# Kernel optimization log

Measured on AMD Instinct MI355X. Metric: run time of the kernel, lower is better.

Reference implementation:

```python
import jax, jax.numpy as jnp
import numpy as np

T, H, W = 365, 256, 256
IN_SZ, HID, OUT_SZ = 2, 64, 1
H_SCALE = 0.1


def setup_inputs() -> dict:
    key = jax.random.key(0)
    ks = jax.random.split(key, 9)
    lim_ih = 1.0 / np.sqrt(HID)
    return {
        "precipitation": jax.random.uniform(ks[0], (T, H, W), dtype=jnp.float32),
        "temperature": jax.random.normal(ks[1], (T, H, W), dtype=jnp.float32),
        "weight_ih": jax.random.uniform(ks[2], (3 * HID, IN_SZ), minval=-lim_ih, maxval=lim_ih, dtype=jnp.float32),
        "weight_hh": jax.random.uniform(ks[3], (3 * HID, HID), minval=-lim_ih, maxval=lim_ih, dtype=jnp.float32),
        "bias": jax.random.uniform(ks[4], (3 * HID,), minval=-lim_ih, maxval=lim_ih, dtype=jnp.float32),
        "bias_n": jax.random.uniform(ks[5], (HID,), minval=-lim_ih, maxval=lim_ih, dtype=jnp.float32),
        "out_w": jax.random.uniform(ks[6], (OUT_SZ, HID), minval=-lim_ih, maxval=lim_ih, dtype=jnp.float32),
        "out_b": jax.random.uniform(ks[7], (OUT_SZ,), minval=-lim_ih, maxval=lim_ih, dtype=jnp.float32),
        "init_h": jax.random.normal(ks[8], (HID,), dtype=jnp.float32) * H_SCALE,
    }


def reference(precipitation, temperature, weight_ih, weight_hh, bias, bias_n, out_w, out_b, init_h):
    t, h, w = temperature.shape
    # (T, N, 2) with N = H*W grid cells treated as batch
    inputs = jnp.stack([precipitation, temperature], axis=-1).reshape(t, h * w, -1)
    h0 = jnp.broadcast_to(init_h, (h * w, init_h.shape[0]))

    def step(hidden, x_t):
        igates = x_t @ weight_ih.T + bias          # (N, 3*HID)
        hgates = hidden @ weight_hh.T              # (N, 3*HID)
        ir, iz, in_ = jnp.split(igates, 3, axis=-1)
        hr, hz, hn = jnp.split(hgates, 3, axis=-1)
        reset = jax.nn.sigmoid(ir + hr)
        update = jax.nn.sigmoid(iz + hz)
        new = jnp.tanh(in_ + reset * (hn + bias_n))
        h_next = new + update * (hidden - new)    # equinox GRUCell convention
        y = (h_next @ out_w.T + out_b)[..., 0]    # (N,)
        return h_next, y

    final_h_flat, smb_flat = jax.lax.scan(step, h0, inputs)
    smb = smb_flat.reshape(t, h, w)
    final_h = final_h_flat.reshape(h, w, -1)
    return smb, final_h
```

## Files before the change

kernel.cpp:

```cpp
#include <hip/hip_runtime.h>

#define T_STEPS 365
#define NCELLS  65536

typedef __attribute__((ext_vector_type(8))) short short8;
typedef __attribute__((ext_vector_type(4))) float f32x4;

static __device__ __forceinline__ short f2bf_rne(float x) {
    union { float f; unsigned u; } v; v.f = x;
    unsigned r = v.u + 0x7fffu + ((v.u >> 16) & 1u);
    return (short)(r >> 16);
}
static __device__ __forceinline__ float bf2f(short b) {
    union { float f; unsigned u; } v; v.u = ((unsigned)(unsigned short)b) << 16;
    return v.f;
}
static __device__ __forceinline__ float fast_rcp(float x) { return __builtin_amdgcn_rcpf(x); }

__global__ __launch_bounds__(256, 2)
void gru_mfma_kernel(const float* __restrict__ precip,
                     const float* __restrict__ temp,
                     const float* __restrict__ w_ih,
                     const float* __restrict__ w_hh,
                     const float* __restrict__ bias,
                     const float* __restrict__ bias_n,
                     const float* __restrict__ out_w,
                     const float* __restrict__ out_b,
                     const float* __restrict__ init_h,
                     float* __restrict__ out)
{
    __shared__ float hbuf[4][16][68];

    const int lane = threadIdx.x & 63;
    const int wid  = threadIdx.x >> 6;
    const int c    = lane & 15;
    const int q    = lane >> 4;
    const int base = (blockIdx.x * 4 + wid) * 16;

    short8 Bf[12][2];
#pragma unroll
    for (int jt = 0; jt < 12; ++jt)
#pragma unroll
        for (int f = 0; f < 2; ++f) {
            const float* src = w_hh + ((16 * jt + c) * 64 + 32 * f + 8 * q);
#pragma unroll
            for (int e = 0; e < 8; ++e) Bf[jt][f][e] = f2bf_rne(src[e]);
        }

    float wr0[4], wr1[4], wz0[4], wz1[4], wn0[4], wn1[4];
    float br[4], bz[4], bn_[4], bnn[4], ow[4];
#pragma unroll
    for (int j = 0; j < 4; ++j) {
        const int u = 16 * j + c;
        wr0[j] = w_ih[2 * u];       wr1[j] = w_ih[2 * u + 1];
        wz0[j] = w_ih[128 + 2 * u]; wz1[j] = w_ih[129 + 2 * u];
        wn0[j] = w_ih[256 + 2 * u]; wn1[j] = w_ih[257 + 2 * u];
        br[j]  = bias[u]; bz[j] = bias[64 + u]; bn_[j] = bias[128 + u];
        bnn[j] = bias_n[u]; ow[j] = out_w[u];
    }
    const float ob = out_b[0];

    float hC[4][4];
#pragma unroll
    for (int j = 0; j < 4; ++j) {
        const float iv = init_h[16 * j + c];
#pragma unroll
        for (int reg = 0; reg < 4; ++reg) hC[j][reg] = iv;
    }
#pragma unroll
    for (int j = 0; j < 4; ++j)
#pragma unroll
        for (int reg = 0; reg < 4; ++reg)
            hbuf[wid][4 * q + reg][16 * j + c] = hC[j][reg];

    const bool selb0 = (c & 1), selb1 = (c & 2);
    const bool do_store = (c < 4);

#pragma unroll 1
    for (int t = 0; t < T_STEPS; ++t) {
        const size_t tofs = (size_t)t * NCELLS + base;
        float pv[4], tv[4];
#pragma unroll
        for (int reg = 0; reg < 4; ++reg) {
            pv[reg] = precip[tofs + 4 * q + reg];
            tv[reg] = temp  [tofs + 4 * q + reg];
        }

        const float* row = &hbuf[wid][c][0];
        f32x4 a0 = *(const f32x4*)(row + 8 * q);
        f32x4 a1 = *(const f32x4*)(row + 8 * q + 4);
        f32x4 a2 = *(const f32x4*)(row + 32 + 8 * q);
        f32x4 a3 = *(const f32x4*)(row + 32 + 8 * q + 4);
        short8 ah0, al0, ah1, al1;
#pragma unroll
        for (int e = 0; e < 4; ++e) {
            short h0 = f2bf_rne(a0[e]); ah0[e]     = h0; al0[e]     = f2bf_rne(a0[e] - bf2f(h0));
            short h1 = f2bf_rne(a1[e]); ah0[4 + e] = h1; al0[4 + e] = f2bf_rne(a1[e] - bf2f(h1));
            short h2 = f2bf_rne(a2[e]); ah1[e]     = h2; al1[e]     = f2bf_rne(a2[e] - bf2f(h2));
            short h3 = f2bf_rne(a3[e]); ah1[4 + e] = h3; al1[4 + e] = f2bf_rne(a3[e] - bf2f(h3));
        }

        f32x4 acc[12];
#pragma unroll
        for (int jt = 0; jt < 12; ++jt) {
            f32x4 a = {0.f, 0.f, 0.f, 0.f};
            a = __builtin_amdgcn_mfma_f32_16x16x32_bf16(ah0, Bf[jt][0], a, 0, 0, 0);
            a = __builtin_amdgcn_mfma_f32_16x16x32_bf16(ah1, Bf[jt][1], a, 0, 0, 0);
            a = __builtin_amdgcn_mfma_f32_16x16x32_bf16(al0, Bf[jt][0], a, 0, 0, 0);
            a = __builtin_amdgcn_mfma_f32_16x16x32_bf16(al1, Bf[jt][1], a, 0, 0, 0);
            acc[jt] = a;
        }

        float psum[4] = {0.f, 0.f, 0.f, 0.f};
#pragma unroll
        for (int j = 0; j < 4; ++j) {
#pragma unroll
            for (int reg = 0; reg < 4; ++reg) {
                const float hr = acc[j][reg];
                const float hz = acc[4 + j][reg];
                const float hn = acc[8 + j][reg];
                const float ir = fmaf(wr0[j], pv[reg], fmaf(wr1[j], tv[reg], br[j]));
                const float iz = fmaf(wz0[j], pv[reg], fmaf(wz1[j], tv[reg], bz[j]));
                const float in_= fmaf(wn0[j], pv[reg], fmaf(wn1[j], tv[reg], bn_[j]));
                const float r  = fast_rcp(1.f + __expf(-(ir + hr)));
                const float z  = fast_rcp(1.f + __expf(-(iz + hz)));
                const float a_ = fmaf(r, hn + bnn[j], in_);
                const float th = 1.f - 2.f * fast_rcp(1.f + __expf(a_ + a_));
                const float hnew = fmaf(z, hC[j][reg] - th, th);
                hC[j][reg] = hnew;
                psum[reg] = fmaf(hnew, ow[j], psum[reg]);
            }
        }

#pragma unroll
        for (int j = 0; j < 4; ++j)
#pragma unroll
            for (int reg = 0; reg < 4; ++reg)
                hbuf[wid][4 * q + reg][16 * j + c] = hC[j][reg];

#pragma unroll
        for (int reg = 0; reg < 4; ++reg) {
            psum[reg] += __shfl_xor(psum[reg], 1);
            psum[reg] += __shfl_xor(psum[reg], 2);
            psum[reg] += __shfl_xor(psum[reg], 4);
            psum[reg] += __shfl_xor(psum[reg], 8);
        }
        float ya = selb0 ? psum[1] : psum[0];
        float yb = selb0 ? psum[3] : psum[2];
        float yv = selb1 ? yb : ya;
        if (do_store) out[tofs + 4 * q + c] = yv + ob;
    }

    const size_t fofs = (size_t)T_STEPS * NCELLS + (size_t)base * 64;
#pragma unroll
    for (int j = 0; j < 4; ++j)
#pragma unroll
        for (int reg = 0; reg < 4; ++reg)
            out[fofs + (size_t)(4 * q + reg) * 64 + 16 * j + c] = hC[j][reg];
}

extern "C" void kernel_launch(void* const* d_in, const int* in_sizes, int n_in,
                              void* d_out, int out_size, void* d_ws, size_t ws_size,
                              hipStream_t stream) {
    const float* precip = (const float*)d_in[0];
    const float* temp   = (const float*)d_in[1];
    const float* w_ih   = (const float*)d_in[2];
    const float* w_hh   = (const float*)d_in[3];
    const float* bias   = (const float*)d_in[4];
    const float* bias_n = (const float*)d_in[5];
    const float* out_w  = (const float*)d_in[6];
    const float* out_b  = (const float*)d_in[7];
    const float* init_h = (const float*)d_in[8];

    gru_mfma_kernel<<<NCELLS / 64, 256, 0, stream>>>(
        precip, temp, w_ih, w_hh, bias, bias_n, out_w, out_b, init_h,
        (float*)d_out);
}
```

Before: 2.405 ms.

## Move W_hh fragments to LDS and fold input gates into MFMA

The W_hh bf16 fragments are no longer held in registers. They are now read each step from shared memory, which frees VGPRs so launch bounds can ask for 3 blocks per SM instead of 2. The r and z input projections plus their biases are folded into an extra MFMA per tile. It uses an augmented A operand (precip/temp hi-lo split and a constant 1.0) with a packed B of w_ih and a bias hi/lo pair, replacing per-element FMAs. The cost is extra LDS reads and one extra MFMA per r/z tile each timestep, plus some precision change from bf16 splitting of the input weights.

```diff
diff --git a/kernel.cpp b/kernel.cpp
--- a/kernel.cpp
+++ b/kernel.cpp
@@ -5,6 +5,7 @@
 
 typedef __attribute__((ext_vector_type(8))) short short8;
 typedef __attribute__((ext_vector_type(4))) float f32x4;
+typedef __attribute__((ext_vector_type(4))) unsigned int u32x4;
 
 static __device__ __forceinline__ short f2bf_rne(float x) {
     union { float f; unsigned u; } v; v.f = x;
@@ -15,9 +16,12 @@
     union { float f; unsigned u; } v; v.u = ((unsigned)(unsigned short)b) << 16;
     return v.f;
 }
+static __device__ __forceinline__ unsigned pack2(short lo, short hi) {
+    return ((unsigned)(unsigned short)lo) | (((unsigned)(unsigned short)hi) << 16);
+}
 static __device__ __forceinline__ float fast_rcp(float x) { return __builtin_amdgcn_rcpf(x); }
 
-__global__ __launch_bounds__(256, 2)
+__global__ __launch_bounds__(256, 3)
 void gru_mfma_kernel(const float* __restrict__ precip,
                      const float* __restrict__ temp,
                      const float* __restrict__ w_ih,
@@ -29,34 +33,48 @@
                      const float* __restrict__ init_h,
                      float* __restrict__ out)
 {
+    __shared__ u32x4 Bfrag[1536];
+    __shared__ u32x4 BExt[256];
     __shared__ float hbuf[4][16][68];
 
-    const int lane = threadIdx.x & 63;
-    const int wid  = threadIdx.x >> 6;
+    const int tid  = threadIdx.x;
+    const int lane = tid & 63;
+    const int wid  = tid >> 6;
     const int c    = lane & 15;
     const int q    = lane >> 4;
     const int base = (blockIdx.x * 4 + wid) * 16;
 
-    short8 Bf[12][2];
-#pragma unroll
-    for (int jt = 0; jt < 12; ++jt)
-#pragma unroll
-        for (int f = 0; f < 2; ++f) {
-            const float* src = w_hh + ((16 * jt + c) * 64 + 32 * f + 8 * q);
-#pragma unroll
-            for (int e = 0; e < 8; ++e) Bf[jt][f][e] = f2bf_rne(src[e]);
-        }
-
-    float wr0[4], wr1[4], wz0[4], wz1[4], wn0[4], wn1[4];
-    float br[4], bz[4], bn_[4], bnn[4], ow[4];
+    for (int idx = tid; idx < 1536; idx += 256) {
+        const int l = idx & 63, jtf = idx >> 6;
+        const int jt = jtf >> 1, f = jtf & 1;
+        const float* src = w_hh + ((16 * jt + (l & 15)) * 64 + 32 * f + 8 * (l >> 4));
+        u32x4 d;
+#pragma unroll
+        for (int p2 = 0; p2 < 4; ++p2)
+            d[p2] = pack2(f2bf_rne(src[2 * p2]), f2bf_rne(src[2 * p2 + 1]));
+        Bfrag[idx] = d;
+    }
+    if (tid < 128) {
+        const int jt = tid >> 4, cc = tid & 15;
+        const int g = 16 * jt + cc;
+        const float b = bias[g];
+        const short bh = f2bf_rne(b);
+        const short bl = f2bf_rne(b - bf2f(bh));
+        u32x4 d;
+        d[0] = pack2(f2bf_rne(w_ih[2 * g]), f2bf_rne(w_ih[2 * g + 1]));
+        d[1] = pack2(bh, bl);
+        d[2] = d[0];
+        d[3] = 0u;
+        BExt[tid] = d;
+        BExt[128 + tid] = u32x4{0u, 0u, 0u, 0u};
+    }
+
+    float wn0[4], wn1[4], bn_[4], bnn[4], ow[4];
 #pragma unroll
     for (int j = 0; j < 4; ++j) {
         const int u = 16 * j + c;
-        wr0[j] = w_ih[2 * u];       wr1[j] = w_ih[2 * u + 1];
-        wz0[j] = w_ih[128 + 2 * u]; wz1[j] = w_ih[129 + 2 * u];
         wn0[j] = w_ih[256 + 2 * u]; wn1[j] = w_ih[257 + 2 * u];
-        br[j]  = bias[u]; bz[j] = bias[64 + u]; bn_[j] = bias[128 + u];
-        bnn[j] = bias_n[u]; ow[j] = out_w[u];
+        bn_[j] = bias[128 + u]; bnn[j] = bias_n[u]; ow[j] = out_w[u];
     }
     const float ob = out_b[0];
 
@@ -72,6 +90,12 @@
 #pragma unroll
         for (int reg = 0; reg < 4; ++reg)
             hbuf[wid][4 * q + reg][16 * j + c] = hC[j][reg];
+
+    __syncthreads();
+
+    const u32x4* extp = BExt + ((q == 0) ? c : 128);
+    const u32x4* bfl  = Bfrag + lane;
+    const unsigned amask = (q == 0) ? 0xFFFFFFFFu : 0u;
 
     const bool selb0 = (c & 1), selb1 = (c & 2);
     const bool do_store = (c < 4);
@@ -85,6 +109,8 @@
             pv[reg] = precip[tofs + 4 * q + reg];
             tv[reg] = temp  [tofs + 4 * q + reg];
         }
+        const float pc = precip[tofs + c];
+        const float tc = temp  [tofs + c];
 
         const float* row = &hbuf[wid][c][0];
         f32x4 a0 = *(const f32x4*)(row + 8 * q);
@@ -100,14 +126,33 @@
             short h3 = f2bf_rne(a3[e]); ah1[4 + e] = h3; al1[4 + e] = f2bf_rne(a3[e] - bf2f(h3));
         }
 
+        const short pch = f2bf_rne(pc), tch = f2bf_rne(tc);
+        const short pcl = f2bf_rne(pc - bf2f(pch)), tcl = f2bf_rne(tc - bf2f(tch));
+        union { u32x4 u; short8 s; } aeu;
+        aeu.u[0] = pack2(pch, tch) & amask;
+        aeu.u[1] = 0x3F803F80u & amask;
+        aeu.u[2] = pack2(pcl, tcl) & amask;
+        aeu.u[3] = 0u;
+        const short8 aext = aeu.s;
+
         f32x4 acc[12];
+        const f32x4 zero4 = {0.f, 0.f, 0.f, 0.f};
 #pragma unroll
         for (int jt = 0; jt < 12; ++jt) {
-            f32x4 a = {0.f, 0.f, 0.f, 0.f};
-            a = __builtin_amdgcn_mfma_f32_16x16x32_bf16(ah0, Bf[jt][0], a, 0, 0, 0);
-            a = __builtin_amdgcn_mfma_f32_16x16x32_bf16(ah1, Bf[jt][1], a, 0, 0, 0);
-            a = __builtin_amdgcn_mfma_f32_16x16x32_bf16(al0, Bf[jt][0], a, 0, 0, 0);
-            a = __builtin_amdgcn_mfma_f32_16x16x32_bf16(al1, Bf[jt][1], a, 0, 0, 0);
+            union { u32x4 u; short8 s; } b0, b1;
+            b0.u = bfl[2 * jt * 64];
+            b1.u = bfl[(2 * jt + 1) * 64];
+            f32x4 a;
+            if (jt < 8) {
+                union { u32x4 u; short8 s; } be; be.u = extp[jt * 16];
+                a = __builtin_amdgcn_mfma_f32_16x16x32_bf16(aext, be.s, zero4, 0, 0, 0);
+            } else {
+                a = zero4;
+            }
+            a = __builtin_amdgcn_mfma_f32_16x16x32_bf16(ah0, b0.s, a, 0, 0, 0);
+            a = __builtin_amdgcn_mfma_f32_16x16x32_bf16(ah1, b1.s, a, 0, 0, 0);
+            a = __builtin_amdgcn_mfma_f32_16x16x32_bf16(al0, b0.s, a, 0, 0, 0);
+            a = __builtin_amdgcn_mfma_f32_16x16x32_bf16(al1, b1.s, a, 0, 0, 0);
             acc[jt] = a;
         }
 
@@ -116,16 +161,14 @@
         for (int j = 0; j < 4; ++j) {
 #pragma unroll
             for (int reg = 0; reg < 4; ++reg) {
-                const float hr = acc[j][reg];
-                const float hz = acc[4 + j][reg];
+                const float xr = acc[j][reg];
+                const float xz = acc[4 + j][reg];
                 const float hn = acc[8 + j][reg];
-                const float ir = fmaf(wr0[j], pv[reg], fmaf(wr1[j], tv[reg], br[j]));
-                const float iz = fmaf(wz0[j], pv[reg], fmaf(wz1[j], tv[reg], bz[j]));
-                const float in_= fmaf(wn0[j], pv[reg], fmaf(wn1[j], tv[reg], bn_[j]));
-                const float r  = fast_rcp(1.f + __expf(-(ir + hr)));
-                const float z  = fast_rcp(1.f + __expf(-(iz + hz)));
+                const float in_ = fmaf(wn0[j], pv[reg], fmaf(wn1[j], tv[reg], bn_[j]));
+                const float r  = fast_rcp(1.f + __expf(-xr));
+                const float z  = fast_rcp(1.f + __expf(-xz));
                 const float a_ = fmaf(r, hn + bnn[j], in_);
-                const float th = 1.f - 2.f * fast_rcp(1.f + __expf(a_ + a_));
+                const float th = fmaf(-2.f, fast_rcp(1.f + __expf(a_ + a_)), 1.f);
                 const float hnew = fmaf(z, hC[j][reg] - th, th);
                 hC[j][reg] = hnew;
                 psum[reg] = fmaf(hnew, ow[j], psum[reg]);
```

After: 5.681 ms. 136% more time.
